# Optimization experiments

Measured on AMD Instinct MI355X. Metric: run time of the kernel, lower is better.

## Reference

```python
import jax, jax.numpy as jnp
import numpy as np

NUM_HEADS = 16
ROPE_BASE = 10000.0


def _apply_rope(x):
    # x: [b, h, l, d]; interleaved-pair RoPE (lucidrains rotate_queries_or_keys)
    b, h, l, d = x.shape
    half = d // 2
    inv_freq = 1.0 / (ROPE_BASE ** (jnp.arange(0, half, dtype=jnp.float32) * 2.0 / d))
    t = jnp.arange(l, dtype=jnp.float32)
    freqs = t[:, None] * inv_freq[None, :]          # [l, d/2]
    cos = jnp.repeat(jnp.cos(freqs), 2, axis=-1)    # [l, d]
    sin = jnp.repeat(jnp.sin(freqs), 2, axis=-1)
    x1 = x[..., ::2]
    x2 = x[..., 1::2]
    rot = jnp.stack([-x2, x1], axis=-1).reshape(x.shape)  # rotate_half, interleaved
    return x * cos + rot * sin


def setup_inputs() -> dict:
    key = jax.random.key(0)
    ks = jax.random.split(key, 8)
    B, L, D = 4, 2048, 1024
    inp = {
        'q': jax.random.normal(ks[0], (B, L, D), dtype=jnp.float32),
        'k': jax.random.normal(ks[1], (B, L, D), dtype=jnp.float32),
        'v': jax.random.normal(ks[2], (B, L, D), dtype=jnp.float32),
        'Wq': jax.random.normal(ks[3], (D, D), dtype=jnp.float32) * 0.02,
        'bq': jnp.zeros((D,), dtype=jnp.float32),
        'Wk': jax.random.normal(ks[4], (D, D), dtype=jnp.float32) * 0.02,
        'bk': jnp.zeros((D,), dtype=jnp.float32),
        'Wv': jax.random.normal(ks[5], (D, D), dtype=jnp.float32) * 0.02,
        'bv': jnp.zeros((D,), dtype=jnp.float32),
        'Wo': jax.random.normal(ks[6], (D, D), dtype=jnp.float32) * 0.02,
        'bo': jnp.zeros((D,), dtype=jnp.float32),
    }
    return inp


def reference(q, k, v, Wq, bq, Wk, bk, Wv, bv, Wo, bo):
    B, L, D = q.shape
    H = NUM_HEADS
    hd = D // H

    def proj(x, W, b):
        y = x @ W.T + b                       # nn.Linear: x W^T + b
        return y.reshape(B, L, H, hd).transpose(0, 2, 1, 3)  # b h l d

    qh = _apply_rope(proj(q, Wq, bq))
    kh = _apply_rope(proj(k, Wk, bk))
    vh = proj(v, Wv, bv)

    scores = jnp.einsum('bhld,bhtd->bhlt', qh, kh) / jnp.sqrt(jnp.float32(hd))
    causal_mask = jnp.tril(jnp.ones((L, L), dtype=bool))
    scores = jnp.where(causal_mask, scores, -jnp.inf)
    probs = jax.nn.softmax(scores, axis=-1)
    attn = jnp.einsum('bhlt,bhtd->bhld', probs, vh)
    attn = attn.transpose(0, 2, 1, 3).reshape(B, L, D)  # b l (h d)
    return attn @ Wo.T + bo
```

## Files before the change

### kernel.cpp

```cpp
#include <hip/hip_runtime.h>
#include <stdint.h>

typedef __attribute__((ext_vector_type(8))) short bf16x8;
typedef __attribute__((ext_vector_type(4))) float f32x4;
typedef __attribute__((ext_vector_type(8))) unsigned short u16x8;
typedef __attribute__((ext_vector_type(4))) unsigned short u16x4;
typedef unsigned short ushort_t;

#define MFMA16(a, b, c) __builtin_amdgcn_mfma_f32_16x16x32_bf16((a), (b), (c), 0, 0, 0)
#define GLDS(g, l)                                                              \
  __builtin_amdgcn_global_load_lds((const __attribute__((address_space(1))) void*)(g), \
                                   (__attribute__((address_space(3))) void*)(l), 16, 0, 0)

static __device__ __forceinline__ unsigned short f2bf(float x) {
  unsigned int u = __builtin_bit_cast(unsigned int, x);
  u += 0x7fff + ((u >> 16) & 1);
  return (unsigned short)(u >> 16);
}

static __device__ __forceinline__ unsigned cvtpk_bf16(float lo, float hi) {
  unsigned r;
  asm("v_cvt_pk_bf16_f32 %0, %1, %2" : "=v"(r) : "v"(lo), "v"(hi));
  return r;
}

__global__ __launch_bounds__(256)
void prep(const float* __restrict__ q, const float* __restrict__ k,
          const float* __restrict__ v, const float* __restrict__ Wq,
          const float* __restrict__ Wk, const float* __restrict__ Wv,
          const float* __restrict__ Wo, ushort_t* __restrict__ oq,
          ushort_t* __restrict__ ok, ushort_t* __restrict__ ov,
          ushort_t* __restrict__ oWq, ushort_t* __restrict__ oWk,
          ushort_t* __restrict__ oWv, ushort_t* __restrict__ oWo,
          float2* __restrict__ tab) {
  const int bid = blockIdx.x;
  if (bid < 14336) {
    const float* in;
    ushort_t* out;
    int lb;
    if (bid < 12288) {
      in = bid < 4096 ? q : (bid < 8192 ? k : v);
      out = bid < 4096 ? oq : (bid < 8192 ? ok : ov);
      lb = bid & 4095;
    } else {
      const int r = bid - 12288;
      in = r < 512 ? Wq : (r < 1024 ? Wk : (r < 1536 ? Wv : Wo));
      out = r < 512 ? oWq : (r < 1024 ? oWk : (r < 1536 ? oWv : oWo));
      lb = r & 511;
    }
    const size_t i = ((size_t)lb * 256 + threadIdx.x) * 8;
    f32x4 a = *(const f32x4*)(in + i);
    f32x4 b = *(const f32x4*)(in + i + 4);
    u16x8 o;
    o[0] = f2bf(a[0]); o[1] = f2bf(a[1]); o[2] = f2bf(a[2]); o[3] = f2bf(a[3]);
    o[4] = f2bf(b[0]); o[5] = f2bf(b[1]); o[6] = f2bf(b[2]); o[7] = f2bf(b[3]);
    *(u16x8*)(out + i) = o;
  } else {
    const int i = (bid - 14336) * 256 + threadIdx.x;
    const int l = i >> 5, f = i & 31;
    float inv = powf(10000.0f, -(float)f / 32.0f);
    float ang = (float)l * inv;
    float s, c;
    sincosf(ang, &s, &c);
    tab[i] = make_float2(c, s);
  }
}

__global__ __launch_bounds__(256, 4)
void gemm_qkv(const ushort_t* __restrict__ qb, const ushort_t* __restrict__ kb2,
              const ushort_t* __restrict__ vb, const ushort_t* __restrict__ Wqb,
              const ushort_t* __restrict__ Wkb, const ushort_t* __restrict__ Wvb,
              const float* __restrict__ bq, const float* __restrict__ bk,
              const float* __restrict__ bv, ushort_t* __restrict__ Qh,
              ushort_t* __restrict__ Kh, ushort_t* __restrict__ VhT,
              const float2* __restrict__ rope) {
  constexpr int K = 1024;
  __shared__ ushort_t As[128 * 64];
  __shared__ ushort_t Bs[128 * 64];

  const int b = blockIdx.x;
  const int xcd = b & 7, i2 = b >> 3;
  const int bx = i2 & 7;
  const int by = ((i2 >> 3) & 7) * 8 + xcd;
  const int z = i2 >> 6;

  const ushort_t* Am = z == 0 ? qb : (z == 1 ? kb2 : vb);
  const ushort_t* Wm = z == 0 ? Wqb : (z == 1 ? Wkb : Wvb);
  const float* bias = z == 0 ? bq : (z == 1 ? bk : bv);
  const float scale = z == 0 ? 0.125f : 1.0f;

  const int t = threadIdx.x;
  const int lane = t & 63, w = t >> 6;
  const int lq = lane & 15, lg = lane >> 4;
  const int wr = w >> 1, wc = w & 1;
  const int row0 = by * 128;
  const int col0 = bx * 128;

  f32x4 acc[4][4] = {};
  for (int kt = 0; kt < K / 64; ++kt) {
    __syncthreads();
#pragma unroll
    for (int it = 0; it < 4; ++it) {
      const int s = it * 256 + t;
      const int ldsoff = (it * 256 + w * 64) * 8;
      GLDS(Am + (size_t)(row0 + (s >> 3)) * K + kt * 64 + (s & 7) * 8, &As[ldsoff]);
      GLDS(Wm + (size_t)(col0 + (s >> 3)) * K + kt * 64 + (s & 7) * 8, &Bs[ldsoff]);
    }
    __syncthreads();
#pragma unroll
    for (int kc = 0; kc < 2; ++kc) {
      bf16x8 af[4], bfr[4];
#pragma unroll
      for (int mf = 0; mf < 4; ++mf)
        af[mf] = *(const bf16x8*)(&As[(wr * 64 + mf * 16 + lq) * 64 + kc * 32 + lg * 8]);
#pragma unroll
      for (int nf = 0; nf < 4; ++nf)
        bfr[nf] = *(const bf16x8*)(&Bs[(wc * 64 + nf * 16 + lq) * 64 + kc * 32 + lg * 8]);
#pragma unroll
      for (int mf = 0; mf < 4; ++mf)
#pragma unroll
        for (int nf = 0; nf < 4; ++nf)
          acc[mf][nf] = MFMA16(af[mf], bfr[nf], acc[mf][nf]);
    }
  }

  float bvv[4];
#pragma unroll
  for (int nf = 0; nf < 4; ++nf) bvv[nf] = bias[col0 + wc * 64 + nf * 16 + lq];

#pragma unroll
  for (int mf = 0; mf < 4; ++mf) {
#pragma unroll
    for (int nf = 0; nf < 4; ++nf) {
      const int col = col0 + wc * 64 + nf * 16 + lq;
      const int h = col >> 6, d = col & 63;
      if (z < 2) {
        ushort_t* o = z == 0 ? Qh : Kh;
#pragma unroll
        for (int u = 0; u < 4; ++u) {
          const int row = row0 + wr * 64 + mf * 16 + 4 * lg + u;
          const int bb = row >> 11, l = row & 2047;
          float val = acc[mf][nf][u] + bvv[nf];
          float2 cs = rope[l * 32 + (d >> 1)];
          float p = __shfl_xor(val, 1, 64);
          val = ((d & 1) ? (val * cs.x + p * cs.y) : (val * cs.x - p * cs.y)) * scale;
          o[(((size_t)bb * 16 + h) * 2048 + l) * 64 + d] = f2bf(val);
        }
      } else {
        const int row = row0 + wr * 64 + mf * 16 + 4 * lg;
        const int bb = row >> 11, l0 = row & 2047;
        u16x4 o;
#pragma unroll
        for (int u = 0; u < 4; ++u) o[u] = f2bf(acc[mf][nf][u] + bvv[nf]);
        *(u16x4*)(VhT + (((size_t)bb * 16 + h) * 64 + d) * 2048 + l0) = o;
      }
    }
  }
}

__global__ __launch_bounds__(256, 4)
void gemm_out(const ushort_t* __restrict__ Am, const ushort_t* __restrict__ Wm,
              const float* __restrict__ bias, float* __restrict__ outp) {
  constexpr int K = 1024;
  __shared__ ushort_t As[128 * 64];
  __shared__ ushort_t Bs[128 * 64];

  const int b = blockIdx.x;
  const int xcd = b & 7, i2 = b >> 3;
  const int bx = i2 & 7;
  const int by = ((i2 >> 3) & 7) * 8 + xcd;

  const int t = threadIdx.x;
  const int lane = t & 63, w = t >> 6;
  const int lq = lane & 15, lg = lane >> 4;
  const int wr = w >> 1, wc = w & 1;
  const int row0 = by * 128;
  const int col0 = bx * 128;

  f32x4 acc[4][4] = {};
  for (int kt = 0; kt < K / 64; ++kt) {
    __syncthreads();
#pragma unroll
    for (int it = 0; it < 4; ++it) {
      const int s = it * 256 + t;
      const int ldsoff = (it * 256 + w * 64) * 8;
      GLDS(Am + (size_t)(row0 + (s >> 3)) * K + kt * 64 + (s & 7) * 8, &As[ldsoff]);
      GLDS(Wm + (size_t)(col0 + (s >> 3)) * K + kt * 64 + (s & 7) * 8, &Bs[ldsoff]);
    }
    __syncthreads();
#pragma unroll
    for (int kc = 0; kc < 2; ++kc) {
      bf16x8 af[4], bfr[4];
#pragma unroll
      for (int mf = 0; mf < 4; ++mf)
        af[mf] = *(const bf16x8*)(&As[(wr * 64 + mf * 16 + lq) * 64 + kc * 32 + lg * 8]);
#pragma unroll
      for (int nf = 0; nf < 4; ++nf)
        bfr[nf] = *(const bf16x8*)(&Bs[(wc * 64 + nf * 16 + lq) * 64 + kc * 32 + lg * 8]);
#pragma unroll
      for (int mf = 0; mf < 4; ++mf)
#pragma unroll
        for (int nf = 0; nf < 4; ++nf)
          acc[mf][nf] = MFMA16(af[mf], bfr[nf], acc[mf][nf]);
    }
  }

  float bvv[4];
#pragma unroll
  for (int nf = 0; nf < 4; ++nf) bvv[nf] = bias[col0 + wc * 64 + nf * 16 + lq];

#pragma unroll
  for (int mf = 0; mf < 4; ++mf) {
#pragma unroll
    for (int nf = 0; nf < 4; ++nf) {
      const int col = col0 + wc * 64 + nf * 16 + lq;
#pragma unroll
      for (int u = 0; u < 4; ++u) {
        const int row = row0 + wr * 64 + mf * 16 + 4 * lg + u;
        outp[(size_t)row * 1024 + col] = acc[mf][nf][u] + bvv[nf];
      }
    }
  }
}

__global__ __launch_bounds__(256, 4)
void attn_fwd(const ushort_t* __restrict__ Qh, const ushort_t* __restrict__ Kh,
              const ushort_t* __restrict__ VhT, ushort_t* __restrict__ attn) {
  constexpr int L = 2048;
  __shared__ __align__(16) char KV[2][16384];
  __shared__ __align__(16) char Pl[4][2048];
  const int t = threadIdx.x;
  const int lane = t & 63, w = t >> 6;
  const int lq = lane & 15, lg = lane >> 4;

  const int fid = blockIdx.y * 16 + blockIdx.x;
  const int bh = (fid & 7) * 8 + (fid >> 7);
  const int i = (fid >> 3) & 15;
  const int lo = i, hi = 31 - i, nt = 32 - i;
  const int qlo = lo * 64 + w * 16 + lq;
  const int qhi = hi * 64 + w * 16 + lq;

  bf16x8 qfl[2], qfh[2];
  {
    const ushort_t* p = Qh + ((size_t)bh * L + qlo) * 64 + lg * 8;
    qfl[0] = *(const bf16x8*)p;
    qfl[1] = *(const bf16x8*)(p + 32);
    const ushort_t* p2 = Qh + ((size_t)bh * L + qhi) * 64 + lg * 8;
    qfh[0] = *(const bf16x8*)p2;
    qfh[1] = *(const bf16x8*)(p2 + 32);
  }

  float ml = -1e30f, ll = 0.0f, mh = -1e30f, lh = 0.0f;
  f32x4 otl[4] = {}, oth[4] = {};
  char* const pw = Pl[w];

  auto STAGE = [&](int bb, int kb) {
    const int kv0 = kb * 64;
#pragma unroll
    for (int it = 0; it < 2; ++it) {
      const int s = it * 256 + t;
      const int r = s >> 3;
      const int sc = (s ^ r) & 7;
      char* base = KV[bb] + (it * 256 + w * 64) * 16;
      GLDS(Kh + ((size_t)bh * L + kv0 + r) * 64 + sc * 8, base);
      GLDS(VhT + ((size_t)bh * 64 + r) * L + kv0 + sc * 8, base + 8192);
    }
  };

  auto TILE = [&](int bb, int kb, int diagkb, int qrow, const bf16x8* qf, float& m,
                  float& lsum, f32x4* ot) {
    const char* Kb = KV[bb];
    const char* Vb = KV[bb] + 8192;
    f32x4 st[4];
    __builtin_amdgcn_s_setprio(1);
#pragma unroll
    for (int kf = 0; kf < 4; ++kf) {
      f32x4 c = {};
#pragma unroll
      for (int kc = 0; kc < 2; ++kc) {
        const int r = kf * 16 + lq;
        const int byte = (r * 128 + kc * 64 + lg * 16) ^ ((r & 7) << 4);
        c = MFMA16(*(const bf16x8*)(Kb + byte), qf[kc], c);
      }
      st[kf] = c;
    }
    __builtin_amdgcn_s_setprio(0);
    if (kb == diagkb) {
      const int kv0 = kb * 64;
#pragma unroll
      for (int kf = 0; kf < 4; ++kf)
#pragma unroll
        for (int u = 0; u < 4; ++u)
          if (kv0 + kf * 16 + 4 * lg + u > qrow) st[kf][u] = -1e30f;
    }
    float pmax = st[0][0];
#pragma unroll
    for (int kf = 0; kf < 4; ++kf)
#pragma unroll
      for (int u = 0; u < 4; ++u) pmax = fmaxf(pmax, st[kf][u]);
    pmax = fmaxf(pmax, __shfl_xor(pmax, 16, 64));
    pmax = fmaxf(pmax, __shfl_xor(pmax, 32, 64));
    if (!__all(pmax <= m + 11.0f)) {
      const float mn = fmaxf(m, pmax);
      const float c2 = __expf(m - mn);
      lsum *= c2;
#pragma unroll
      for (int df = 0; df < 4; ++df) ot[df] *= c2;
      m = mn;
    }
    float psum = 0.0f;
#pragma unroll
    for (int kf = 0; kf < 4; ++kf) {
      const float p0 = __expf(st[kf][0] - m);
      const float p1 = __expf(st[kf][1] - m);
      const float p2 = __expf(st[kf][2] - m);
      const float p3 = __expf(st[kf][3] - m);
      psum += (p0 + p1) + (p2 + p3);
      uint2 pk;
      pk.x = cvtpk_bf16(p0, p1);
      pk.y = cvtpk_bf16(p2, p3);
      const int byte = (lq * 128 + kf * 32 + lg * 8) ^ ((lq & 7) << 4);
      *(uint2*)(pw + byte) = pk;
    }
    psum += __shfl_xor(psum, 16, 64);
    psum += __shfl_xor(psum, 32, 64);
    lsum += psum;
    asm volatile("s_waitcnt lgkmcnt(0)" ::: "memory");
    __builtin_amdgcn_s_setprio(1);
#pragma unroll
    for (int df = 0; df < 4; ++df) {
#pragma unroll
      for (int kc = 0; kc < 2; ++kc) {
        const int r = df * 16 + lq;
        const int byte = (r * 128 + kc * 64 + lg * 16) ^ ((r & 7) << 4);
        const int pbyte = (lq * 128 + kc * 64 + lg * 16) ^ ((lq & 7) << 4);
        ot[df] = MFMA16(*(const bf16x8*)(Vb + byte), *(const bf16x8*)(pw + pbyte), ot[df]);
      }
    }
    __builtin_amdgcn_s_setprio(0);
  };

  STAGE(0, 0);
  __syncthreads();
  int cur = 0;
  for (int kb = 0; kb < nt; ++kb) {
    if (kb + 1 < nt) STAGE(cur ^ 1, kb + 1);
    TILE(cur, kb, hi, qhi, qfh, mh, lh, oth);
    if (kb <= lo) TILE(cur, kb, lo, qlo, qfl, ml, ll, otl);
    __syncthreads();
    cur ^= 1;
  }

  const int b = bh >> 4, h = bh & 15;
  {
    const float inv = 1.0f / lh;
#pragma unroll
    for (int df = 0; df < 4; ++df) {
      u16x4 o;
#pragma unroll
      for (int u = 0; u < 4; ++u) o[u] = f2bf(oth[df][u] * inv);
      *(u16x4*)(attn + ((size_t)b * L + qhi) * 1024 + h * 64 + df * 16 + 4 * lg) = o;
    }
  }
  {
    const float inv = 1.0f / ll;
#pragma unroll
    for (int df = 0; df < 4; ++df) {
      u16x4 o;
#pragma unroll
      for (int u = 0; u < 4; ++u) o[u] = f2bf(otl[df][u] * inv);
      *(u16x4*)(attn + ((size_t)b * L + qlo) * 1024 + h * 64 + df * 16 + 4 * lg) = o;
    }
  }
}

extern "C" void kernel_launch(void* const* d_in, const int* in_sizes, int n_in,
                              void* d_out, int out_size, void* d_ws, size_t ws_size,
                              hipStream_t stream) {
  const float* q = (const float*)d_in[0];
  const float* k = (const float*)d_in[1];
  const float* v = (const float*)d_in[2];
  const float* Wq = (const float*)d_in[3];
  const float* bq = (const float*)d_in[4];
  const float* Wk = (const float*)d_in[5];
  const float* bk = (const float*)d_in[6];
  const float* Wv = (const float*)d_in[7];
  const float* bv = (const float*)d_in[8];
  const float* Wo = (const float*)d_in[9];
  const float* bo = (const float*)d_in[10];

  char* ws = (char*)d_ws;
  const size_t MB = 1ull << 20;
  ushort_t* qb = (ushort_t*)(ws + 0 * MB);
  ushort_t* kb = (ushort_t*)(ws + 16 * MB);
  ushort_t* vb = (ushort_t*)(ws + 32 * MB);
  ushort_t* Wqb = (ushort_t*)(ws + 48 * MB);
  ushort_t* Wkb = (ushort_t*)(ws + 50 * MB);
  ushort_t* Wvb = (ushort_t*)(ws + 52 * MB);
  ushort_t* Wob = (ushort_t*)(ws + 54 * MB);
  float2* rope = (float2*)(ws + 56 * MB);
  ushort_t* Qh = (ushort_t*)(ws + 57 * MB);
  ushort_t* Kh = (ushort_t*)(ws + 73 * MB);
  ushort_t* VhT = (ushort_t*)(ws + 89 * MB);
  ushort_t* attnb = qb;

  prep<<<14592, 256, 0, stream>>>(q, k, v, Wq, Wk, Wv, Wo, qb, kb, vb, Wqb, Wkb, Wvb,
                                  Wob, rope);

  gemm_qkv<<<1536, 256, 0, stream>>>(qb, kb, vb, Wqb, Wkb, Wvb, bq, bk, bv, Qh, Kh, VhT,
                                     rope);

  attn_fwd<<<dim3(16, 64), 256, 0, stream>>>(Qh, Kh, VhT, attnb);

  gemm_out<<<512, 256, 0, stream>>>(attnb, Wob, bo, (float*)d_out);

  (void)in_sizes; (void)n_in; (void)out_size; (void)ws_size;
}
```

Before: 191.8 us.

## Triple-buffer QKV GEMM with swizzled LDS and larger 256x128 tiles

Rewrites the QKV projection GEMM main loop as a 3-stage global->LDS pipeline using vmcnt-based waits and a single barrier per k-step, replacing the two-syncthreads load-then-compute pattern. Block tile grows to 256x128 with 512 threads and the grid is halved. An XOR swizzle on LDS addresses targets bank conflicts, and setprio wraps the MFMA burst. The intent is to hide global load latency behind MFMA work. The cost is much larger LDS use (~144KB) and occupancy of one block per CU.

Result: slower. 202.7 us (+5.7%).

```diff
diff --git a/kernel.cpp b/kernel.cpp
--- a/kernel.cpp
+++ b/kernel.cpp
@@ -66,7 +66,7 @@
   }
 }
 
-__global__ __launch_bounds__(256, 4)
+__global__ __launch_bounds__(512, 1)
 void gemm_qkv(const ushort_t* __restrict__ qb, const ushort_t* __restrict__ kb2,
               const ushort_t* __restrict__ vb, const ushort_t* __restrict__ Wqb,
               const ushort_t* __restrict__ Wkb, const ushort_t* __restrict__ Wvb,
@@ -75,14 +75,16 @@
               ushort_t* __restrict__ Kh, ushort_t* __restrict__ VhT,
               const float2* __restrict__ rope) {
   constexpr int K = 1024;
-  __shared__ ushort_t As[128 * 64];
-  __shared__ ushort_t Bs[128 * 64];
+  constexpr int NT = K / 64;
+  __shared__ ushort_t As[3][256 * 64];
+  __shared__ ushort_t Bs[3][128 * 64];
 
   const int b = blockIdx.x;
   const int xcd = b & 7, i2 = b >> 3;
   const int bx = i2 & 7;
-  const int by = ((i2 >> 3) & 7) * 8 + xcd;
-  const int z = i2 >> 6;
+  const int byh = (i2 >> 3) & 3;
+  const int z = i2 >> 5;
+  const int by = byh * 8 + xcd;
 
   const ushort_t* Am = z == 0 ? qb : (z == 1 ? kb2 : vb);
   const ushort_t* Wm = z == 0 ? Wqb : (z == 1 ? Wkb : Wvb);
@@ -93,34 +95,69 @@
   const int lane = t & 63, w = t >> 6;
   const int lq = lane & 15, lg = lane >> 4;
   const int wr = w >> 1, wc = w & 1;
-  const int row0 = by * 128;
+  const int row0 = by * 256;
   const int col0 = bx * 128;
 
+  auto STAGE = [&](int buf, int kt) {
+#pragma unroll
+    for (int r = 0; r < 4; ++r) {
+      const int s = r * 512 + t;
+      const int sc = (s ^ (s >> 3)) & 7;
+      GLDS(Am + (size_t)(row0 + (s >> 3)) * K + kt * 64 + sc * 8,
+           &As[buf][(r * 512 + w * 64) * 8]);
+    }
+#pragma unroll
+    for (int r = 0; r < 2; ++r) {
+      const int s = r * 512 + t;
+      const int sc = (s ^ (s >> 3)) & 7;
+      GLDS(Wm + (size_t)(col0 + (s >> 3)) * K + kt * 64 + sc * 8,
+           &Bs[buf][(r * 512 + w * 64) * 8]);
+    }
+  };
+
   f32x4 acc[4][4] = {};
-  for (int kt = 0; kt < K / 64; ++kt) {
-    __syncthreads();
-#pragma unroll
-    for (int it = 0; it < 4; ++it) {
-      const int s = it * 256 + t;
-      const int ldsoff = (it * 256 + w * 64) * 8;
-      GLDS(Am + (size_t)(row0 + (s >> 3)) * K + kt * 64 + (s & 7) * 8, &As[ldsoff]);
-      GLDS(Wm + (size_t)(col0 + (s >> 3)) * K + kt * 64 + (s & 7) * 8, &Bs[ldsoff]);
-    }
-    __syncthreads();
+  STAGE(0, 0);
+  STAGE(1, 1);
+  asm volatile("s_waitcnt vmcnt(6)" ::: "memory");
+  __builtin_amdgcn_sched_barrier(0);
+  __builtin_amdgcn_s_barrier();
+  __builtin_amdgcn_sched_barrier(0);
+
+  for (int kt = 0; kt < NT; ++kt) {
+    const int buf = kt % 3;
+    if (kt + 2 < NT) STAGE((kt + 2) % 3, kt + 2);
+    const char* Ab = (const char*)&As[buf][0];
+    const char* Bb = (const char*)&Bs[buf][0];
 #pragma unroll
     for (int kc = 0; kc < 2; ++kc) {
       bf16x8 af[4], bfr[4];
 #pragma unroll
-      for (int mf = 0; mf < 4; ++mf)
-        af[mf] = *(const bf16x8*)(&As[(wr * 64 + mf * 16 + lq) * 64 + kc * 32 + lg * 8]);
-#pragma unroll
-      for (int nf = 0; nf < 4; ++nf)
-        bfr[nf] = *(const bf16x8*)(&Bs[(wc * 64 + nf * 16 + lq) * 64 + kc * 32 + lg * 8]);
+      for (int mf = 0; mf < 4; ++mf) {
+        const int ar = wr * 64 + mf * 16 + lq;
+        af[mf] = *(const bf16x8*)(Ab + ((ar * 128 + kc * 64 + lg * 16) ^ ((ar & 7) << 4)));
+      }
+#pragma unroll
+      for (int nf = 0; nf < 4; ++nf) {
+        const int br = wc * 64 + nf * 16 + lq;
+        bfr[nf] = *(const bf16x8*)(Bb + ((br * 128 + kc * 64 + lg * 16) ^ ((br & 7) << 4)));
+      }
+      __builtin_amdgcn_s_setprio(1);
 #pragma unroll
       for (int mf = 0; mf < 4; ++mf)
 #pragma unroll
         for (int nf = 0; nf < 4; ++nf)
           acc[mf][nf] = MFMA16(af[mf], bfr[nf], acc[mf][nf]);
+      __builtin_amdgcn_s_setprio(0);
+    }
+    if (kt <= NT - 3) {
+      asm volatile("s_waitcnt vmcnt(6)" ::: "memory");
+    } else if (kt == NT - 2) {
+      asm volatile("s_waitcnt vmcnt(0)" ::: "memory");
+    }
+    if (kt < NT - 1) {
+      __builtin_amdgcn_sched_barrier(0);
+      __builtin_amdgcn_s_barrier();
+      __builtin_amdgcn_sched_barrier(0);
     }
   }
 
@@ -407,8 +444,8 @@
   prep<<<14592, 256, 0, stream>>>(q, k, v, Wq, Wk, Wv, Wo, qb, kb, vb, Wqb, Wkb, Wvb,
                                   Wob, rope);
 
-  gemm_qkv<<<1536, 256, 0, stream>>>(qb, kb, vb, Wqb, Wkb, Wvb, bq, bk, bv, Qh, Kh, VhT,
-                                     rope);
+  gemm_qkv<<<768, 512, 0, stream>>>(qb, kb, vb, Wqb, Wkb, Wvb, bq, bk, bv, Qh, Kh, VhT,
+                                    rope);
 
   attn_fwd<<<dim3(16, 64), 256, 0, stream>>>(Qh, Kh, VhT, attnb);
 
```
